# Performance work log

Measured on AMD Instinct MI355X. Metric: run time of the kernel, lower is better.

The kernel has to match this reference:

```python
import jax, jax.numpy as jnp
import numpy as np

D_LOGIC = 256
D_MEMORY = 256
NHEAD = 4
B, S = 2, 4096


def setup_inputs() -> dict:
    key = jax.random.key(0)
    ks = jax.random.split(key, 12)
    scale = 0.02
    x_logic = jax.random.normal(ks[0], (B, S, D_LOGIC), dtype=jnp.float32)
    x_memory = jax.random.normal(ks[1], (B, S, D_MEMORY), dtype=jnp.float32)
    mask = jax.random.randint(ks[2], (1, 1, S, S), 0, 2, dtype=jnp.int32)
    # torch nn.Linear weights are [out_features, in_features]
    Wq = jax.random.normal(ks[3], (D_LOGIC, D_LOGIC), dtype=jnp.float32) * scale
    bq = jnp.zeros((D_LOGIC,), dtype=jnp.float32)
    Wk = jax.random.normal(ks[4], (D_LOGIC, D_LOGIC), dtype=jnp.float32) * scale
    bk = jnp.zeros((D_LOGIC,), dtype=jnp.float32)
    Wv = jax.random.normal(ks[5], (D_MEMORY, D_MEMORY), dtype=jnp.float32) * scale
    bv = jnp.zeros((D_MEMORY,), dtype=jnp.float32)
    Wo = jax.random.normal(ks[6], (D_MEMORY, D_MEMORY), dtype=jnp.float32) * scale
    bo = jnp.zeros((D_MEMORY,), dtype=jnp.float32)
    return {"x_logic": x_logic, "x_memory": x_memory, "mask": mask,
            "Wq": Wq, "bq": bq, "Wk": Wk, "bk": bk,
            "Wv": Wv, "bv": bv, "Wo": Wo, "bo": bo}


def reference(x_logic, x_memory, mask, Wq, bq, Wk, bk, Wv, bv, Wo, bo):
    batch, seq, _ = x_logic.shape
    hd_l = D_LOGIC // NHEAD   # head_dim_logic
    hd_m = D_MEMORY // NHEAD  # head_dim_memory
    # Q, K from logic stream
    Q = (x_logic @ Wq.T + bq).reshape(batch, seq, NHEAD, hd_l)
    K = (x_logic @ Wk.T + bk).reshape(batch, seq, NHEAD, hd_l)
    # scores: [B, H, S, S]
    scores = jnp.einsum('bqhd,bkhd->bhqk', Q, K) / jnp.sqrt(jnp.float32(hd_l))
    scores = jnp.where(mask == 0, jnp.float32(-1e9), scores)
    attn = jax.nn.softmax(scores, axis=-1)
    # V from memory stream
    V = (x_memory @ Wv.T + bv).reshape(batch, seq, NHEAD, hd_m)
    out = jnp.einsum('bhqk,bkhd->bqhd', attn, V).reshape(batch, seq, D_MEMORY)
    return out @ Wo.T + bo
```

## Files before the change

### kernel.cpp

```cpp
#include <hip/hip_runtime.h>

#define S_  4096
#define HD_ 64
#define H_  4
#define B_  2
#define DM  256
#define NS  2
#define KSPAN (S_ / NS)
#define NITER (KSPAN / 64)

typedef __bf16 bf16x8 __attribute__((ext_vector_type(8)));
typedef __bf16 bf16x4 __attribute__((ext_vector_type(4)));
typedef float  f32x4  __attribute__((ext_vector_type(4)));
typedef unsigned long long u64;

__global__ __launch_bounds__(256) void prep_kernel(const int* __restrict__ mask,
                                                   u64* __restrict__ packed,
                                                   const float* __restrict__ Wq,
                                                   const float* __restrict__ Wk,
                                                   const float* __restrict__ Wv,
                                                   const float* __restrict__ Wo,
                                                   __bf16* __restrict__ wqb,
                                                   __bf16* __restrict__ wkb,
                                                   __bf16* __restrict__ wvb,
                                                   __bf16* __restrict__ wob) {
    const int bid = blockIdx.x;
    if (bid < 1024) {
        const int gw   = bid * 4 + (threadIdx.x >> 6);
        const int lane = threadIdx.x & 63;
        for (int step = 0; step < 64; ++step) {
            const int wi  = gw + step * 4096;
            const int kbb = wi >> 12;
            const int q   = wi & (S_ - 1);
            const int mv  = mask[(size_t)q * S_ + kbb * 64 + lane];
            const u64 bits = __ballot(mv != 0);
            if (lane == 0) packed[wi] = bits;
        }
    } else {
        const int t = (bid - 1024) * 256 + threadIdx.x;
        for (int i = t; i < 65536; i += 16384) {
            const int arr = i >> 14, idx = i & 16383;
            const float* src = arr == 0 ? Wq : arr == 1 ? Wk : arr == 2 ? Wv : Wo;
            __bf16* dst      = arr == 0 ? wqb : arr == 1 ? wkb : arr == 2 ? wvb : wob;
            float4 v = reinterpret_cast<const float4*>(src)[idx];
            bf16x4 o = { (__bf16)v.x, (__bf16)v.y, (__bf16)v.z, (__bf16)v.w };
            reinterpret_cast<bf16x4*>(dst)[idx] = o;
        }
    }
}

__global__ __launch_bounds__(256) void proj_qkv_kernel(const float* __restrict__ xl,
                                                       const float* __restrict__ xm,
                                                       const __bf16* __restrict__ wq,
                                                       const __bf16* __restrict__ wk,
                                                       const __bf16* __restrict__ wv,
                                                       const float* __restrict__ bq,
                                                       const float* __restrict__ bk,
                                                       const float* __restrict__ bv,
                                                       __bf16* __restrict__ Qb,
                                                       __bf16* __restrict__ Kb,
                                                       __bf16* __restrict__ Vtb) {
    const int mode = blockIdx.y;
    const float*  X    = (mode == 2) ? xm : xl;
    const __bf16* W    = (mode == 0) ? wq : (mode == 1) ? wk : wv;
    const float*  bias = (mode == 0) ? bq : (mode == 1) ? bk : bv;
    const float scale  = (mode == 0) ? 0.18033688011112042f : 1.0f;

    const int wid  = threadIdx.x >> 6;
    const int lane = threadIdx.x & 63;
    const int g = lane >> 4, c = lane & 15;
    const int m0 = blockIdx.x * 64 + wid * 16;
    const float* Xp = X + (size_t)m0 * DM;

    f32x4 acc[16];
#pragma unroll
    for (int i = 0; i < 16; ++i) acc[i] = (f32x4){0.f, 0.f, 0.f, 0.f};

#pragma unroll
    for (int kf = 0; kf < 8; ++kf) {
        const float* ap = Xp + c * DM + kf * 32 + g * 8;
        float4 u0 = *reinterpret_cast<const float4*>(ap);
        float4 u1 = *reinterpret_cast<const float4*>(ap + 4);
        bf16x8 a = { (__bf16)u0.x, (__bf16)u0.y, (__bf16)u0.z, (__bf16)u0.w,
                     (__bf16)u1.x, (__bf16)u1.y, (__bf16)u1.z, (__bf16)u1.w };
#pragma unroll
        for (int nt = 0; nt < 16; ++nt) {
            bf16x8 b = *reinterpret_cast<const bf16x8*>(W + (size_t)(nt * 16 + c) * DM + kf * 32 + g * 8);
            acc[nt] = __builtin_amdgcn_mfma_f32_16x16x32_bf16(a, b, acc[nt], 0, 0, 0);
        }
    }

#pragma unroll
    for (int nt = 0; nt < 16; ++nt) {
        const int n = nt * 16 + c;
        const float bs = bias[n];
        const int h = n >> 6, d = n & 63;
#pragma unroll
        for (int r = 0; r < 4; ++r) {
            const int m = m0 + g * 4 + r;
            const float v = (acc[nt][r] + bs) * scale;
            const int b_ = m >> 12, s = m & (S_ - 1);
            if (mode == 0)
                Qb[((size_t)(b_ * H_ + h) * S_ + s) * HD_ + d] = (__bf16)v;
            else if (mode == 1)
                Kb[((size_t)(b_ * H_ + h) * S_ + s) * HD_ + d] = (__bf16)v;
            else
                Vtb[((size_t)(b_ * H_ + h) * HD_ + d) * S_ + s] = (__bf16)v;
        }
    }
}

__global__ __launch_bounds__(256, 4) void attn_kernel(const __bf16* __restrict__ Q,
                                                      const __bf16* __restrict__ K,
                                                      const __bf16* __restrict__ Vt,
                                                      const u64* __restrict__ packed,
                                                      float* __restrict__ Opart,
                                                      float* __restrict__ Lpart) {
    __shared__ __bf16 Kt[64][72];
    __shared__ __bf16 Vl[64][72];
    __shared__ __bf16 Pl[4][16][72];

    const int bh = blockIdx.x;
    const int sp = blockIdx.y;
    const int qt = blockIdx.z;
    const int tid  = threadIdx.x;
    const int wid  = tid >> 6;
    const int lane = tid & 63;
    const int g = lane >> 4, c = lane & 15;
    const int q0w = qt * 64 + wid * 16;

    const __bf16* Qp = Q + ((size_t)bh * S_ + q0w) * HD_;
    bf16x8 qb0 = *reinterpret_cast<const bf16x8*>(Qp + c * HD_ + g * 8);
    bf16x8 qb1 = *reinterpret_cast<const bf16x8*>(Qp + c * HD_ + 32 + g * 8);

    const __bf16* Kp = K  + (size_t)bh * S_ * HD_;
    const __bf16* Vp = Vt + (size_t)bh * HD_ * S_;

    const int srow = tid >> 2;
    const int sseg = (tid & 3) * 16;

    f32x4 o[4];
#pragma unroll
    for (int i = 0; i < 4; ++i) o[i] = (f32x4){0.f, 0.f, 0.f, 0.f};
    float rs = 0.f;

    const int k0 = sp * KSPAN;

    bf16x8 kr0, kr1, vr0, vr1;
    {
        const __bf16* krow = Kp + (size_t)(k0 + srow) * HD_ + sseg;
        const __bf16* vrow = Vp + (size_t)srow * S_ + k0 + sseg;
        kr0 = *reinterpret_cast<const bf16x8*>(krow);
        kr1 = *reinterpret_cast<const bf16x8*>(krow + 8);
        vr0 = *reinterpret_cast<const bf16x8*>(vrow);
        vr1 = *reinterpret_cast<const bf16x8*>(vrow + 8);
        *reinterpret_cast<bf16x8*>(&Kt[srow][sseg])     = kr0;
        *reinterpret_cast<bf16x8*>(&Kt[srow][sseg + 8]) = kr1;
        *reinterpret_cast<bf16x8*>(&Vl[srow][sseg])     = vr0;
        *reinterpret_cast<bf16x8*>(&Vl[srow][sseg + 8]) = vr1;
    }
    __syncthreads();

    for (int it = 0; it < NITER; ++it) {
        const int kb = k0 + it * 64;
        const bool more = (it + 1 < NITER);
        if (more) {
            const __bf16* krow = Kp + (size_t)(kb + 64 + srow) * HD_ + sseg;
            const __bf16* vrow = Vp + (size_t)srow * S_ + kb + 64 + sseg;
            kr0 = *reinterpret_cast<const bf16x8*>(krow);
            kr1 = *reinterpret_cast<const bf16x8*>(krow + 8);
            vr0 = *reinterpret_cast<const bf16x8*>(vrow);
            vr1 = *reinterpret_cast<const bf16x8*>(vrow + 8);
        }

        const u64 mw = packed[(size_t)(kb >> 6) * S_ + q0w + c];
        const unsigned wlo = (unsigned)mw, whi = (unsigned)(mw >> 32);

        f32x4 st[4];
#pragma unroll
        for (int nt = 0; nt < 4; ++nt) {
            bf16x8 ka0 = *reinterpret_cast<const bf16x8*>(&Kt[nt * 16 + c][g * 8]);
            bf16x8 ka1 = *reinterpret_cast<const bf16x8*>(&Kt[nt * 16 + c][32 + g * 8]);
            f32x4 z = (f32x4){0.f, 0.f, 0.f, 0.f};
            st[nt] = __builtin_amdgcn_mfma_f32_16x16x32_bf16(ka0, qb0, z, 0, 0, 0);
            st[nt] = __builtin_amdgcn_mfma_f32_16x16x32_bf16(ka1, qb1, st[nt], 0, 0, 0);
        }

#pragma unroll
        for (int nt = 0; nt < 4; ++nt) {
            const unsigned w = (nt < 2) ? wlo : whi;
            const unsigned base = (nt & 1) * 16 + g * 4;
            float p0 = ((w >> (base + 0)) & 1u) ? exp2f(st[nt][0]) : 0.f;
            float p1 = ((w >> (base + 1)) & 1u) ? exp2f(st[nt][1]) : 0.f;
            float p2 = ((w >> (base + 2)) & 1u) ? exp2f(st[nt][2]) : 0.f;
            float p3 = ((w >> (base + 3)) & 1u) ? exp2f(st[nt][3]) : 0.f;
            rs += (p0 + p1) + (p2 + p3);
            bf16x4 pw = { (__bf16)p0, (__bf16)p1, (__bf16)p2, (__bf16)p3 };
            *reinterpret_cast<bf16x4*>(&Pl[wid][c][nt * 16 + g * 4]) = pw;
        }

        bf16x8 pa0 = *reinterpret_cast<const bf16x8*>(&Pl[wid][c][g * 8]);
        bf16x8 pa1 = *reinterpret_cast<const bf16x8*>(&Pl[wid][c][32 + g * 8]);

#pragma unroll
        for (int nt = 0; nt < 4; ++nt) {
            bf16x8 vb0 = *reinterpret_cast<const bf16x8*>(&Vl[nt * 16 + c][g * 8]);
            bf16x8 vb1 = *reinterpret_cast<const bf16x8*>(&Vl[nt * 16 + c][32 + g * 8]);
            o[nt] = __builtin_amdgcn_mfma_f32_16x16x32_bf16(pa0, vb0, o[nt], 0, 0, 0);
            o[nt] = __builtin_amdgcn_mfma_f32_16x16x32_bf16(pa1, vb1, o[nt], 0, 0, 0);
        }

        __syncthreads();
        if (more) {
            *reinterpret_cast<bf16x8*>(&Kt[srow][sseg])     = kr0;
            *reinterpret_cast<bf16x8*>(&Kt[srow][sseg + 8]) = kr1;
            *reinterpret_cast<bf16x8*>(&Vl[srow][sseg])     = vr0;
            *reinterpret_cast<bf16x8*>(&Vl[srow][sseg + 8]) = vr1;
            __syncthreads();
        }
    }

    rs += __shfl_xor(rs, 16);
    rs += __shfl_xor(rs, 32);
    if (lane < 16)
        Lpart[(size_t)(bh * NS + sp) * S_ + q0w + c] = rs;

    const size_t obase = ((size_t)(bh * NS + sp) * S_ + q0w) * 64;
#pragma unroll
    for (int nt = 0; nt < 4; ++nt) {
#pragma unroll
        for (int r = 0; r < 4; ++r)
            Opart[obase + (size_t)(g * 4 + r) * 64 + nt * 16 + c] = o[nt][r];
    }
}

__global__ __launch_bounds__(256) void proj_o_kernel(const float* __restrict__ Opart,
                                                     const float* __restrict__ Lpart,
                                                     const __bf16* __restrict__ wo,
                                                     const float* __restrict__ bo,
                                                     float* __restrict__ out) {
    const int wid  = threadIdx.x >> 6;
    const int lane = threadIdx.x & 63;
    const int g = lane >> 4, c = lane & 15;
    const int m0 = blockIdx.x * 64 + wid * 16;

    const int row = m0 + c;
    const int b_ = row >> 12, s = row & (S_ - 1);

    f32x4 acc[16];
#pragma unroll
    for (int i = 0; i < 16; ++i) acc[i] = (f32x4){0.f, 0.f, 0.f, 0.f};

#pragma unroll
    for (int kf = 0; kf < 8; ++kf) {
        const int dcol = kf * 32 + g * 8;
        const int h = dcol >> 6, dm = dcol & 63;
        const int bh = b_ * H_ + h;
        const float l = Lpart[(size_t)(bh * NS + 0) * S_ + s] +
                        Lpart[(size_t)(bh * NS + 1) * S_ + s];
        const float invl = 1.0f / l;
        const size_t base0 = ((size_t)(bh * NS + 0) * S_ + s) * 64 + dm;
        const size_t base1 = ((size_t)(bh * NS + 1) * S_ + s) * 64 + dm;
        float4 p00 = *reinterpret_cast<const float4*>(Opart + base0);
        float4 p01 = *reinterpret_cast<const float4*>(Opart + base0 + 4);
        float4 p10 = *reinterpret_cast<const float4*>(Opart + base1);
        float4 p11 = *reinterpret_cast<const float4*>(Opart + base1 + 4);
        bf16x8 a = { (__bf16)((p00.x + p10.x) * invl), (__bf16)((p00.y + p10.y) * invl),
                     (__bf16)((p00.z + p10.z) * invl), (__bf16)((p00.w + p10.w) * invl),
                     (__bf16)((p01.x + p11.x) * invl), (__bf16)((p01.y + p11.y) * invl),
                     (__bf16)((p01.z + p11.z) * invl), (__bf16)((p01.w + p11.w) * invl) };
#pragma unroll
        for (int nt = 0; nt < 16; ++nt) {
            bf16x8 b = *reinterpret_cast<const bf16x8*>(wo + (size_t)(nt * 16 + c) * DM + kf * 32 + g * 8);
            acc[nt] = __builtin_amdgcn_mfma_f32_16x16x32_bf16(a, b, acc[nt], 0, 0, 0);
        }
    }

#pragma unroll
    for (int nt = 0; nt < 16; ++nt) {
        const int n = nt * 16 + c;
        const float bs = bo[n];
#pragma unroll
        for (int r = 0; r < 4; ++r) {
            const int m = m0 + g * 4 + r;
            out[(size_t)m * DM + n] = acc[nt][r] + bs;
        }
    }
}

extern "C" void kernel_launch(void* const* d_in, const int* in_sizes, int n_in,
                              void* d_out, int out_size, void* d_ws, size_t ws_size,
                              hipStream_t stream) {
    const float* x_logic  = (const float*)d_in[0];
    const float* x_memory = (const float*)d_in[1];
    const int*   mask     = (const int*)d_in[2];
    const float* Wq = (const float*)d_in[3];
    const float* bq = (const float*)d_in[4];
    const float* Wk = (const float*)d_in[5];
    const float* bk = (const float*)d_in[6];
    const float* Wv = (const float*)d_in[7];
    const float* bv = (const float*)d_in[8];
    const float* Wo = (const float*)d_in[9];
    const float* bo = (const float*)d_in[10];
    float* out = (float*)d_out;

    char* ws = (char*)d_ws;
    size_t off = 0;
    auto alloc = [&](size_t bytes) { char* p = ws + off; off += (bytes + 255) & ~255ull; return p; };

    const size_t NX = (size_t)B_ * S_ * DM;
    __bf16* wqb = (__bf16*)alloc((size_t)DM * DM * 2);
    __bf16* wkb = (__bf16*)alloc((size_t)DM * DM * 2);
    __bf16* wvb = (__bf16*)alloc((size_t)DM * DM * 2);
    __bf16* wob = (__bf16*)alloc((size_t)DM * DM * 2);
    u64*    packed = (u64*)alloc((size_t)S_ * (S_ / 64) * 8);
    __bf16* Qb  = (__bf16*)alloc(NX * 2);
    __bf16* Kb  = (__bf16*)alloc(NX * 2);
    __bf16* Vtb = (__bf16*)alloc(NX * 2);
    float*  Opart = (float*)alloc((size_t)B_ * H_ * NS * S_ * HD_ * 4);
    float*  Lpart = (float*)alloc((size_t)B_ * H_ * NS * S_ * 4);

    prep_kernel<<<1088, 256, 0, stream>>>(mask, packed, Wq, Wk, Wv, Wo, wqb, wkb, wvb, wob);
    proj_qkv_kernel<<<dim3(128, 3), 256, 0, stream>>>(x_logic, x_memory, wqb, wkb, wvb,
                                                      bq, bk, bv, Qb, Kb, Vtb);
    attn_kernel<<<dim3(8, NS, 64), 256, 0, stream>>>(Qb, Kb, Vtb, packed, Opart, Lpart);
    proj_o_kernel<<<128, 256, 0, stream>>>(Opart, Lpart, wob, bo, out);
}
```

Measured before the change: 161.9 us.

## Fuse prep with QKV projection, widen attention blocks, split keys four ways

Merges the mask-packing kernel and the QKV projection into one launch, dropping the separate weight-to-bf16 pass so weights are converted inline from fp32. The attention kernel now runs 512 threads (8 waves, 128 queries) per block, with K and V tile loads split between the two thread halves. The key-split count rises from 2 to 4, and partial outputs are stored as bf16 instead of fp32. This saves a kernel launch and intermediate traffic and raises attention parallelism, at the cost of redundant weight conversion per block, a larger reduction in the output projection, and lower precision in the partial sums.

```diff
diff --git a/kernel.cpp b/kernel.cpp
--- a/kernel.cpp
+++ b/kernel.cpp
@@ -5,7 +5,7 @@
 #define H_  4
 #define B_  2
 #define DM  256
-#define NS  2
+#define NS  4
 #define KSPAN (S_ / NS)
 #define NITER (KSPAN / 64)
 
@@ -14,16 +14,27 @@
 typedef float  f32x4  __attribute__((ext_vector_type(4)));
 typedef unsigned long long u64;
 
-__global__ __launch_bounds__(256) void prep_kernel(const int* __restrict__ mask,
-                                                   u64* __restrict__ packed,
-                                                   const float* __restrict__ Wq,
-                                                   const float* __restrict__ Wk,
-                                                   const float* __restrict__ Wv,
-                                                   const float* __restrict__ Wo,
-                                                   __bf16* __restrict__ wqb,
-                                                   __bf16* __restrict__ wkb,
-                                                   __bf16* __restrict__ wvb,
-                                                   __bf16* __restrict__ wob) {
+__device__ __forceinline__ bf16x8 cvt8(const float* p) {
+    float4 u0 = *reinterpret_cast<const float4*>(p);
+    float4 u1 = *reinterpret_cast<const float4*>(p + 4);
+    bf16x8 r = { (__bf16)u0.x, (__bf16)u0.y, (__bf16)u0.z, (__bf16)u0.w,
+                 (__bf16)u1.x, (__bf16)u1.y, (__bf16)u1.z, (__bf16)u1.w };
+    return r;
+}
+
+__global__ __launch_bounds__(256) void prep_proj_kernel(const int* __restrict__ mask,
+                                                        u64* __restrict__ packed,
+                                                        const float* __restrict__ xl,
+                                                        const float* __restrict__ xm,
+                                                        const float* __restrict__ Wq,
+                                                        const float* __restrict__ Wk,
+                                                        const float* __restrict__ Wv,
+                                                        const float* __restrict__ bq,
+                                                        const float* __restrict__ bk,
+                                                        const float* __restrict__ bv,
+                                                        __bf16* __restrict__ Qb,
+                                                        __bf16* __restrict__ Kb,
+                                                        __bf16* __restrict__ Vtb) {
     const int bid = blockIdx.x;
     if (bid < 1024) {
         const int gw   = bid * 4 + (threadIdx.x >> 6);
@@ -36,40 +47,20 @@
             const u64 bits = __ballot(mv != 0);
             if (lane == 0) packed[wi] = bits;
         }
-    } else {
-        const int t = (bid - 1024) * 256 + threadIdx.x;
-        for (int i = t; i < 65536; i += 16384) {
-            const int arr = i >> 14, idx = i & 16383;
-            const float* src = arr == 0 ? Wq : arr == 1 ? Wk : arr == 2 ? Wv : Wo;
-            __bf16* dst      = arr == 0 ? wqb : arr == 1 ? wkb : arr == 2 ? wvb : wob;
-            float4 v = reinterpret_cast<const float4*>(src)[idx];
-            bf16x4 o = { (__bf16)v.x, (__bf16)v.y, (__bf16)v.z, (__bf16)v.w };
-            reinterpret_cast<bf16x4*>(dst)[idx] = o;
-        }
-    }
-}
-
-__global__ __launch_bounds__(256) void proj_qkv_kernel(const float* __restrict__ xl,
-                                                       const float* __restrict__ xm,
-                                                       const __bf16* __restrict__ wq,
-                                                       const __bf16* __restrict__ wk,
-                                                       const __bf16* __restrict__ wv,
-                                                       const float* __restrict__ bq,
-                                                       const float* __restrict__ bk,
-                                                       const float* __restrict__ bv,
-                                                       __bf16* __restrict__ Qb,
-                                                       __bf16* __restrict__ Kb,
-                                                       __bf16* __restrict__ Vtb) {
-    const int mode = blockIdx.y;
+        return;
+    }
+    const int pb   = bid - 1024;
+    const int mode = pb >> 7;
+    const int mb   = pb & 127;
     const float*  X    = (mode == 2) ? xm : xl;
-    const __bf16* W    = (mode == 0) ? wq : (mode == 1) ? wk : wv;
+    const float*  W    = (mode == 0) ? Wq : (mode == 1) ? Wk : Wv;
     const float*  bias = (mode == 0) ? bq : (mode == 1) ? bk : bv;
     const float scale  = (mode == 0) ? 0.18033688011112042f : 1.0f;
 
     const int wid  = threadIdx.x >> 6;
     const int lane = threadIdx.x & 63;
     const int g = lane >> 4, c = lane & 15;
-    const int m0 = blockIdx.x * 64 + wid * 16;
+    const int m0 = mb * 64 + wid * 16;
     const float* Xp = X + (size_t)m0 * DM;
 
     f32x4 acc[16];
@@ -78,14 +69,10 @@
 
 #pragma unroll
     for (int kf = 0; kf < 8; ++kf) {
-        const float* ap = Xp + c * DM + kf * 32 + g * 8;
-        float4 u0 = *reinterpret_cast<const float4*>(ap);
-        float4 u1 = *reinterpret_cast<const float4*>(ap + 4);
-        bf16x8 a = { (__bf16)u0.x, (__bf16)u0.y, (__bf16)u0.z, (__bf16)u0.w,
-                     (__bf16)u1.x, (__bf16)u1.y, (__bf16)u1.z, (__bf16)u1.w };
+        bf16x8 a = cvt8(Xp + c * DM + kf * 32 + g * 8);
 #pragma unroll
         for (int nt = 0; nt < 16; ++nt) {
-            bf16x8 b = *reinterpret_cast<const bf16x8*>(W + (size_t)(nt * 16 + c) * DM + kf * 32 + g * 8);
+            bf16x8 b = cvt8(W + (size_t)(nt * 16 + c) * DM + kf * 32 + g * 8);
             acc[nt] = __builtin_amdgcn_mfma_f32_16x16x32_bf16(a, b, acc[nt], 0, 0, 0);
         }
     }
@@ -110,15 +97,15 @@
     }
 }
 
-__global__ __launch_bounds__(256, 4) void attn_kernel(const __bf16* __restrict__ Q,
+__global__ __launch_bounds__(512, 8) void attn_kernel(const __bf16* __restrict__ Q,
                                                       const __bf16* __restrict__ K,
                                                       const __bf16* __restrict__ Vt,
                                                       const u64* __restrict__ packed,
-                                                      float* __restrict__ Opart,
+                                                      __bf16* __restrict__ Opart,
                                                       float* __restrict__ Lpart) {
     __shared__ __bf16 Kt[64][72];
     __shared__ __bf16 Vl[64][72];
-    __shared__ __bf16 Pl[4][16][72];
+    __shared__ __bf16 Pl[8][16][72];
 
     const int bh = blockIdx.x;
     const int sp = blockIdx.y;
@@ -127,7 +114,7 @@
     const int wid  = tid >> 6;
     const int lane = tid & 63;
     const int g = lane >> 4, c = lane & 15;
-    const int q0w = qt * 64 + wid * 16;
+    const int q0w = qt * 128 + wid * 16;
 
     const __bf16* Qp = Q + ((size_t)bh * S_ + q0w) * HD_;
     bf16x8 qb0 = *reinterpret_cast<const bf16x8*>(Qp + c * HD_ + g * 8);
@@ -136,8 +123,14 @@
     const __bf16* Kp = K  + (size_t)bh * S_ * HD_;
     const __bf16* Vp = Vt + (size_t)bh * HD_ * S_;
 
-    const int srow = tid >> 2;
-    const int sseg = (tid & 3) * 16;
+    const bool isK = tid < 256;
+    const int st_  = isK ? tid : tid - 256;
+    const int srow = st_ >> 2;
+    const int sseg = (st_ & 3) * 16;
+    const __bf16* sbase = isK ? (Kp + (size_t)srow * HD_ + sseg)
+                              : (Vp + (size_t)srow * S_ + sseg);
+    const size_t sstep = isK ? (size_t)64 * HD_ : 64;
+    __bf16* sdst = isK ? &Kt[srow][sseg] : &Vl[srow][sseg];
 
     f32x4 o[4];
 #pragma unroll
@@ -145,32 +138,22 @@
     float rs = 0.f;
 
     const int k0 = sp * KSPAN;
-
-    bf16x8 kr0, kr1, vr0, vr1;
-    {
-        const __bf16* krow = Kp + (size_t)(k0 + srow) * HD_ + sseg;
-        const __bf16* vrow = Vp + (size_t)srow * S_ + k0 + sseg;
-        kr0 = *reinterpret_cast<const bf16x8*>(krow);
-        kr1 = *reinterpret_cast<const bf16x8*>(krow + 8);
-        vr0 = *reinterpret_cast<const bf16x8*>(vrow);
-        vr1 = *reinterpret_cast<const bf16x8*>(vrow + 8);
-        *reinterpret_cast<bf16x8*>(&Kt[srow][sseg])     = kr0;
-        *reinterpret_cast<bf16x8*>(&Kt[srow][sseg + 8]) = kr1;
-        *reinterpret_cast<bf16x8*>(&Vl[srow][sseg])     = vr0;
-        *reinterpret_cast<bf16x8*>(&Vl[srow][sseg + 8]) = vr1;
-    }
+    const __bf16* sptr = sbase + (isK ? (size_t)k0 * HD_ : (size_t)k0);
+
+    bf16x8 r0, r1;
+    r0 = *reinterpret_cast<const bf16x8*>(sptr);
+    r1 = *reinterpret_cast<const bf16x8*>(sptr + 8);
+    *reinterpret_cast<bf16x8*>(sdst)     = r0;
+    *reinterpret_cast<bf16x8*>(sdst + 8) = r1;
     __syncthreads();
 
     for (int it = 0; it < NITER; ++it) {
         const int kb = k0 + it * 64;
         const bool more = (it + 1 < NITER);
         if (more) {
-            const __bf16* krow = Kp + (size_t)(kb + 64 + srow) * HD_ + sseg;
-            const __bf16* vrow = Vp + (size_t)srow * S_ + kb + 64 + sseg;
-            kr0 = *reinterpret_cast<const bf16x8*>(krow);
-            kr1 = *reinterpret_cast<const bf16x8*>(krow + 8);
-            vr0 = *reinterpret_cast<const bf16x8*>(vrow);
-            vr1 = *reinterpret_cast<const bf16x8*>(vrow + 8);
+            sptr += sstep;
+            r0 = *reinterpret_cast<const bf16x8*>(sptr);
+            r1 = *reinterpret_cast<const bf16x8*>(sptr + 8);
         }
 
         const u64 mw = packed[(size_t)(kb >> 6) * S_ + q0w + c];
@@ -212,10 +195,8 @@
 
         __syncthreads();
         if (more) {
-            *reinterpret_cast<bf16x8*>(&Kt[srow][sseg])     = kr0;
-            *reinterpret_cast<bf16x8*>(&Kt[srow][sseg + 8]) = kr1;
-            *reinterpret_cast<bf16x8*>(&Vl[srow][sseg])     = vr0;
-            *reinterpret_cast<bf16x8*>(&Vl[srow][sseg + 8]) = vr1;
+            *reinterpret_cast<bf16x8*>(sdst)     = r0;
+            *reinterpret_cast<bf16x8*>(sdst + 8) = r1;
             __syncthreads();
         }
     }
@@ -230,13 +211,13 @@
     for (int nt = 0; nt < 4; ++nt) {
 #pragma unroll
         for (int r = 0; r < 4; ++r)
-            Opart[obase + (size_t)(g * 4 + r) * 64 + nt * 16 + c] = o[nt][r];
-    }
-}
-
-__global__ __launch_bounds__(256) void proj_o_kernel(const float* __restrict__ Opart,
+            Opart[obase + (size_t)(g * 4 + r) * 64 + nt * 16 + c] = (__bf16)o[nt][r];
+    }
+}
+
+__global__ __launch_bounds__(256) void proj_o_kernel(const __bf16* __restrict__ Opart,
                                                      const float* __restrict__ Lpart,
-                                                     const __bf16* __restrict__ wo,
+                                                     const float* __restrict__ Wo,
                                                      const float* __restrict__ bo,
                                                      float* __restrict__ out) {
     const int wid  = threadIdx.x >> 6;
@@ -256,22 +237,24 @@
         const int dcol = kf * 32 + g * 8;
         const int h = dcol >> 6, dm = dcol & 63;
         const int bh = b_ * H_ + h;
-        const float l = Lpart[(size_t)(bh * NS + 0) * S_ + s] +
-                        Lpart[(size_t)(bh * NS + 1) * S_ + s];
+        float l = 0.f;
+        float sum[8] = {0.f, 0.f, 0.f, 0.f, 0.f, 0.f, 0.f, 0.f};
+#pragma unroll
+        for (int sp = 0; sp < NS; ++sp) {
+            l += Lpart[(size_t)(bh * NS + sp) * S_ + s];
+            const size_t base = ((size_t)(bh * NS + sp) * S_ + s) * 64 + dm;
+            bf16x8 p = *reinterpret_cast<const bf16x8*>(Opart + base);
+#pragma unroll
+            for (int j = 0; j < 8; ++j) sum[j] += (float)p[j];
+        }
         const float invl = 1.0f / l;
-        const size_t base0 = ((size_t)(bh * NS + 0) * S_ + s) * 64 + dm;
-        const size_t base1 = ((size_t)(bh * NS + 1) * S_ + s) * 64 + dm;
-        float4 p00 = *reinterpret_cast<const float4*>(Opart + base0);
-        float4 p01 = *reinterpret_cast<const float4*>(Opart + base0 + 4);
-        float4 p10 = *reinterpret_cast<const float4*>(Opart + base1);
-        float4 p11 = *reinterpret_cast<const float4*>(Opart + base1 + 4);
-        bf16x8 a = { (__bf16)((p00.x + p10.x) * invl), (__bf16)((p00.y + p10.y) * invl),
-                     (__bf16)((p00.z + p10.z) * invl), (__bf16)((p00.w + p10.w) * invl),
-                     (__bf16)((p01.x + p11.x) * invl), (__bf16)((p01.y + p11.y) * invl),
-                     (__bf16)((p01.z + p11.z) * invl), (__bf16)((p01.w + p11.w) * invl) };
+        bf16x8 a = { (__bf16)(sum[0] * invl), (__bf16)(sum[1] * invl),
+                     (__bf16)(sum[2] * invl), (__bf16)(sum[3] * invl),
+                     (__bf16)(sum[4] * invl), (__bf16)(sum[5] * invl),
+                     (__bf16)(sum[6] * invl), (__bf16)(sum[7] * invl) };
 #pragma unroll
         for (int nt = 0; nt < 16; ++nt) {
-            bf16x8 b = *reinterpret_cast<const bf16x8*>(wo + (size_t)(nt * 16 + c) * DM + kf * 32 + g * 8);
+            bf16x8 b = cvt8(Wo + (size_t)(nt * 16 + c) * DM + kf * 32 + g * 8);
             acc[nt] = __builtin_amdgcn_mfma_f32_16x16x32_bf16(a, b, acc[nt], 0, 0, 0);
         }
     }
@@ -309,20 +292,15 @@
     auto alloc = [&](size_t bytes) { char* p = ws + off; off += (bytes + 255) & ~255ull; return p; };
 
     const size_t NX = (size_t)B_ * S_ * DM;
-    __bf16* wqb = (__bf16*)alloc((size_t)DM * DM * 2);
-    __bf16* wkb = (__bf16*)alloc((size_t)DM * DM * 2);
-    __bf16* wvb = (__bf16*)alloc((size_t)DM * DM * 2);
-    __bf16* wob = (__bf16*)alloc((size_t)DM * DM * 2);
     u64*    packed = (u64*)alloc((size_t)S_ * (S_ / 64) * 8);
     __bf16* Qb  = (__bf16*)alloc(NX * 2);
     __bf16* Kb  = (__bf16*)alloc(NX * 2);
     __bf16* Vtb = (__bf16*)alloc(NX * 2);
-    float*  Opart = (float*)alloc((size_t)B_ * H_ * NS * S_ * HD_ * 4);
+    __bf16* Opart = (__bf16*)alloc((size_t)B_ * H_ * NS * S_ * HD_ * 2);
     float*  Lpart = (float*)alloc((size_t)B_ * H_ * NS * S_ * 4);
 
-    prep_kernel<<<1088, 256, 0, stream>>>(mask, packed, Wq, Wk, Wv, Wo, wqb, wkb, wvb, wob);
-    proj_qkv_kernel<<<dim3(128, 3), 256, 0, stream>>>(x_logic, x_memory, wqb, wkb, wvb,
-                                                      bq, bk, bv, Qb, Kb, Vtb);
-    attn_kernel<<<dim3(8, NS, 64), 256, 0, stream>>>(Qb, Kb, Vtb, packed, Opart, Lpart);
-    proj_o_kernel<<<128, 256, 0, stream>>>(Opart, Lpart, wob, bo, out);
-}
+    prep_proj_kernel<<<1408, 256, 0, stream>>>(mask, packed, x_logic, x_memory,
+                                               Wq, Wk, Wv, bq, bk, bv, Qb, Kb, Vtb);
+    attn_kernel<<<dim3(8, NS, S_ / 128), 512, 0, stream>>>(Qb, Kb, Vtb, packed, Opart, Lpart);
+    proj_o_kernel<<<128, 256, 0, stream>>>(Opart, Lpart, Wo, bo, out);
+}
```

Result: slower. 307.5 us (+90.0%).
